# Optimization experiments

Hardware: AMD Instinct MI355X
Metric: run time of the kernel (lower is better)

The kernel has to match this reference:

```python
import jax, jax.numpy as jnp
import numpy as np

S, T, B = 50, 50, 64
SRC_V, TRG_V = 36616, 23262
E, EH, DH = 300, 512, 1024


def setup_inputs() -> dict:
    key = jax.random.key(0)
    ks = jax.random.split(key, 20)
    n = lambda k, shape: jax.random.normal(k, shape, jnp.float32) * 0.05
    return {
        "train_src_batch": jax.random.randint(ks[0], (S, B), 0, SRC_V),
        "train_trg_batch": jax.random.randint(ks[1], (T, B), 0, TRG_V),
        "emb_en": n(ks[2], (SRC_V, E)),
        "emb_de": n(ks[3], (TRG_V, E)),
        "enc_W_ih_f": n(ks[4], (4 * EH, E)),
        "enc_W_hh_f": n(ks[5], (4 * EH, EH)),
        "enc_b_f": n(ks[6], (4 * EH,)),
        "enc_W_ih_b": n(ks[7], (4 * EH, E)),
        "enc_W_hh_b": n(ks[8], (4 * EH, EH)),
        "enc_b_b": n(ks[9], (4 * EH,)),
        "dec_W_ih": n(ks[10], (4 * DH, E + DH)),
        "dec_W_hh": n(ks[11], (4 * DH, DH)),
        "dec_b": n(ks[12], (4 * DH,)),
        "W_gen": n(ks[13], (TRG_V, DH)),
        "b_gen": n(ks[14], (TRG_V,)),
        "W_i": n(ks[15], (DH, DH)),
        "W_o": n(ks[16], (DH, 2 * DH)),
    }


def _lstm_step(x, h, c, W_ih, W_hh, b):
    # PyTorch gate order: i, f, g, o
    gates = x @ W_ih.T + h @ W_hh.T + b
    i, f, g, o = jnp.split(gates, 4, axis=-1)
    c_new = jax.nn.sigmoid(f) * c + jax.nn.sigmoid(i) * jnp.tanh(g)
    h_new = jax.nn.sigmoid(o) * jnp.tanh(c_new)
    return h_new, c_new


def _run_lstm(x_seq, W_ih, W_hh, b, hidden):
    h0 = jnp.zeros((x_seq.shape[1], hidden), x_seq.dtype)
    def step(carry, x):
        h, c = carry
        h, c = _lstm_step(x, h, c, W_ih, W_hh, b)
        return (h, c), h
    (h, c), hs = jax.lax.scan(step, (h0, h0), x_seq)
    return hs, h, c


def _forward(train_src_batch, train_trg_batch, emb_en, emb_de,
             enc_W_ih_f, enc_W_hh_f, enc_b_f, enc_W_ih_b, enc_W_hh_b, enc_b_b,
             dec_W_ih, dec_W_hh, dec_b, W_gen, b_gen, W_i, W_o):
    x = emb_en[train_src_batch]                       # [S,B,E]
    hs_f, hf, cf = _run_lstm(x, enc_W_ih_f, enc_W_hh_f, enc_b_f, EH)
    hs_b, hb, cb = _run_lstm(x[::-1], enc_W_ih_b, enc_W_hh_b, enc_b_b, EH)
    output_hs = jnp.concatenate([hs_f, hs_b[::-1]], axis=-1)  # [S,B,1024]
    # Faithful to h.contiguous().view(B,1024) on direction-major [2,B,512]
    h = jnp.reshape(jnp.stack([hf, hb], axis=0), (B, DH))
    c = jnp.reshape(jnp.stack([cf, cb], axis=0), (B, DH))

    emb_trg = emb_de[train_trg_batch[: T - 1]]        # [T-1,B,E]

    def step(carry, e):
        h, c = carry
        # score[j,b] = output_hs[j,b] . (W_i h[b])  (the diag of the original mm)
        scores = jnp.einsum('sbd,bd->sb', output_hs, h @ W_i.T)
        # legacy nn.Softmax() on 2D input -> softmax over dim=1 (batch axis)
        a = jax.nn.softmax(scores, axis=1)
        s_t = jnp.einsum('sb,sbd->bd', a, output_hs)
        c_t = jnp.tanh(jnp.concatenate([s_t, h], axis=1) @ W_o.T)
        dec_in = jnp.concatenate([c_t, e], axis=1)    # [B, 1024+300]
        h, c = _lstm_step(dec_in, h, c, dec_W_ih, dec_W_hh, dec_b)
        logp = jax.nn.log_softmax(h @ W_gen.T + b_gen, axis=1)
        return (h, c), logp

    _, outs = jax.lax.scan(step, (h, c), emb_trg)     # [T-1,B,V]
    out0 = jnp.zeros((1, B, TRG_V), outs.dtype)       # output[0] filled with 0
    return jnp.concatenate([out0, outs], axis=0)      # [T,B,V]


def reference(train_src_batch, train_trg_batch, emb_en, emb_de,
              enc_W_ih_f, enc_W_hh_f, enc_b_f, enc_W_ih_b, enc_W_hh_b, enc_b_b,
              dec_W_ih, dec_W_hh, dec_b, W_gen, b_gen, W_i, W_o):
    return _forward(train_src_batch, train_trg_batch, emb_en, emb_de,
                    enc_W_ih_f, enc_W_hh_f, enc_b_f, enc_W_ih_b, enc_W_hh_b, enc_b_b,
                    dec_W_ih, dec_W_hh, dec_b, W_gen, b_gen, W_i, W_o)
```

## Files before the change

kernel.cpp:

```cpp
#include <hip/hip_runtime.h>
#include <hip/hip_bf16.h>

#define SS 50
#define TT 50
#define BB 64
#define TRGV 23262
#define EE 300
#define EH 512
#define DH 1024

#define GMRE 3136
#define GMP 3200
#define GK 1024
#define GNRE TRGV
#define GNP 23296

typedef short bf16x8 __attribute__((ext_vector_type(8)));
typedef float f32x4 __attribute__((ext_vector_type(4)));

__device__ __forceinline__ void glds16(const void* g, void* l) {
  __builtin_amdgcn_global_load_lds(
      (const __attribute__((address_space(1))) void*)g,
      (__attribute__((address_space(3))) void*)l, 16, 0, 0);
}

__device__ __forceinline__ float sigm(float x) { return 1.f / (1.f + expf(-x)); }
__device__ __forceinline__ float sum4(f32x4 v) { return v[0] + v[1] + v[2] + v[3]; }
__device__ __forceinline__ float bfu2f(unsigned short u) {
  unsigned int x = ((unsigned)u) << 16;
  return __uint_as_float(x);
}

__device__ __forceinline__ void split2(float x, __hip_bfloat16& hi, __hip_bfloat16& lo) {
  hi = __float2bfloat16(x);
  lo = __float2bfloat16(x - __bfloat162float(hi));
}

__device__ __forceinline__ void gbarg(unsigned* arrive, unsigned* gen,
                                      int idxInGrp, int n, bool poller) {
  __syncthreads();
  unsigned g = __hip_atomic_load(gen, __ATOMIC_RELAXED, __HIP_MEMORY_SCOPE_AGENT);
  if (threadIdx.x == 0)
    __hip_atomic_store(arrive + idxInGrp, g + 1u, __ATOMIC_RELEASE, __HIP_MEMORY_SCOPE_AGENT);
  if (poller) {
    int i = threadIdx.x;
    if (i < n) {
      while (__hip_atomic_load(arrive + i, __ATOMIC_RELAXED, __HIP_MEMORY_SCOPE_AGENT) < g + 1u)
        __builtin_amdgcn_s_sleep(1);
      (void)__hip_atomic_load(arrive + i, __ATOMIC_ACQUIRE, __HIP_MEMORY_SCOPE_AGENT);
    }
    __syncthreads();
    if (threadIdx.x == 0)
      __hip_atomic_store(gen, g + 1u, __ATOMIC_RELEASE, __HIP_MEMORY_SCOPE_AGENT);
  }
  if (threadIdx.x == 0) {
    while (__hip_atomic_load(gen, __ATOMIC_RELAXED, __HIP_MEMORY_SCOPE_AGENT) < g + 1u)
      __builtin_amdgcn_s_sleep(1);
    (void)__hip_atomic_load(gen, __ATOMIC_ACQUIRE, __HIP_MEMORY_SCOPE_AGENT);
  }
  __syncthreads();
}

__global__ void k_zero(float* __restrict__ p, long n) {
  long i = (long)blockIdx.x * 256 + threadIdx.x;
  if (i < n) p[i] = 0.f;
}
__global__ void k_zero_bf(__hip_bfloat16* __restrict__ p, long n) {
  long i = (long)blockIdx.x * 256 + threadIdx.x;
  if (i < n) p[i] = __float2bfloat16(0.f);
}

__global__ void k_embed(const int* __restrict__ src, const float* __restrict__ emb,
                        float* __restrict__ x) {
  int id = blockIdx.x * 256 + threadIdx.x;
  if (id >= SS * BB * EE) return;
  int sb = id / EE, e = id % EE;
  x[id] = emb[(long)src[sb] * EE + e];
}

__global__ void k_dbperm(const float* __restrict__ db, float* __restrict__ dbp) {
  int id = blockIdx.x * 256 + threadIdx.x;
  if (id >= 4096) return;
  int u = id >> 2, g = id & 3;
  dbp[id] = db[g * 1024 + u];
}

__global__ void k_split_pad(const float* __restrict__ in, int ld_in, int col_off,
                            int Kreal, int Kpad, int rows_real, long rows_pad,
                            int mode, __hip_bfloat16* __restrict__ out) {
  long id = (long)blockIdx.x * 256 + threadIdx.x;
  if (id >= rows_pad * Kpad) return;
  long r = id / Kpad;
  int k = id % Kpad;
  float v = 0.f;
  if (r < rows_real && k < Kreal) {
    if (mode == 3) {
      v = in[(long)k * ld_in + col_off + r];
    } else {
      long sr = r;
      if (mode == 1) sr = ((49 - (r >> 6)) << 6) + (r & 63);
      else if (mode == 2) sr = (long)(r & 3) * 1024 + (r >> 2);
      v = in[sr * ld_in + col_off + k];
    }
  }
  __hip_bfloat16 hi, lo;
  split2(v, hi, lo);
  out[r * 2 * Kpad + k] = hi;
  out[r * 2 * Kpad + Kpad + k] = lo;
}

__global__ void k_embgather_split(const int* __restrict__ trg, const float* __restrict__ emb,
                                  __hip_bfloat16* __restrict__ out) {
  long id = (long)blockIdx.x * 256 + threadIdx.x;
  if (id >= 3200L * 320) return;
  long r = id / 320;
  int k = id % 320;
  int t = r >> 6, b = r & 63;
  float v = 0.f;
  if (t < TT - 1 && k < EE) v = emb[(long)trg[t * BB + b] * EE + k];
  __hip_bfloat16 hi, lo;
  split2(v, hi, lo);
  out[r * 640 + k] = hi;
  out[r * 640 + 320 + k] = lo;
}

__global__ void k_tobf16_pad(const float* __restrict__ W, __hip_bfloat16* __restrict__ Wb,
                             long nrow_real, long nrow_pad, int K) {
  long id = (long)blockIdx.x * 256 + threadIdx.x;
  if (id >= nrow_pad * K) return;
  long r = id / K;
  Wb[id] = __float2bfloat16(r < nrow_real ? W[id] : 0.f);
}

__global__ void k_repackT(const float* __restrict__ in, float* __restrict__ out) {
  long id = (long)blockIdx.x * 256 + threadIdx.x;
  if (id >= 3200L * 1024) return;
  long r = id >> 10;
  int n = id & 1023;
  out[((long)(n >> 2) * 3200 + r) * 4 + (n & 3)] = in[id];
}

template<int OUTBF>
__global__ __launch_bounds__(256) void k_gsplit(
    const __hip_bfloat16* __restrict__ A2, const __hip_bfloat16* __restrict__ W2,
    const float* __restrict__ bias, void* __restrict__ Cout,
    int Mreal, int Nreal, int ldc, int Kpad) {
  __shared__ __hip_bfloat16 As[128 * 32];
  __shared__ __hip_bfloat16 Bs[128 * 32];
  int tid = threadIdx.x, lane = tid & 63, w = tid >> 6;
  long m0 = (long)blockIdx.y * 128, n0 = (long)blockIdx.x * 128;
  int lda2 = 2 * Kpad;
  int srow = lane >> 2;
  int scol = (lane & 3) * 8;
  char* lA0 = (char*)As + w * 2048;
  char* lA1 = lA0 + 1024;
  char* lB0 = (char*)Bs + w * 2048;
  char* lB1 = lB0 + 1024;
  int wm = (w >> 1) * 64, wn = (w & 1) * 64;
  int fr = lane & 15;
  int kc = (lane >> 4) * 8;
  f32x4 acc[4][4] = {};

  for (int seg = 0; seg < 3; ++seg) {
    const __hip_bfloat16* Ab = A2 + (seg == 1 ? Kpad : 0);
    const __hip_bfloat16* Wb = W2 + (seg == 2 ? Kpad : 0);
    const __hip_bfloat16* gA0 = Ab + (m0 + w * 32 + srow) * (long)lda2 + scol;
    const __hip_bfloat16* gA1 = gA0 + 16L * lda2;
    const __hip_bfloat16* gB0 = Wb + (n0 + w * 32 + srow) * (long)lda2 + scol;
    const __hip_bfloat16* gB1 = gB0 + 16L * lda2;
    for (int kt = 0; kt < Kpad / 32; ++kt) {
      int k0 = kt * 32;
      glds16(gA0 + k0, lA0);
      glds16(gA1 + k0, lA1);
      glds16(gB0 + k0, lB0);
      glds16(gB1 + k0, lB1);
      __syncthreads();
      bf16x8 a[4], b[4];
      for (int mi = 0; mi < 4; ++mi)
        a[mi] = *(const bf16x8*)(As + (wm + mi * 16 + fr) * 32 + kc);
      for (int ni = 0; ni < 4; ++ni)
        b[ni] = *(const bf16x8*)(Bs + (wn + ni * 16 + fr) * 32 + kc);
      for (int mi = 0; mi < 4; ++mi)
        for (int ni = 0; ni < 4; ++ni)
          acc[mi][ni] = __builtin_amdgcn_mfma_f32_16x16x32_bf16(a[mi], b[ni], acc[mi][ni], 0, 0, 0);
      __syncthreads();
    }
  }

  for (int mi = 0; mi < 4; ++mi) {
    for (int ni = 0; ni < 4; ++ni) {
      int n = (int)n0 + wn + ni * 16 + (lane & 15);
      if (n >= Nreal) continue;
      float bv = bias ? bias[n] : 0.f;
      for (int r = 0; r < 4; ++r) {
        int m = (int)m0 + wm + mi * 16 + (lane >> 4) * 4 + r;
        if (m >= Mreal) continue;
        float v = acc[mi][ni][r] + bv;
        if (OUTBF) ((__hip_bfloat16*)Cout)[(long)m * ldc + n] = __float2bfloat16(v);
        else ((float*)Cout)[(long)m * ldc + n] = v;
      }
    }
  }
}

__global__ __launch_bounds__(512) void persist_enc(
    const float* __restrict__ xW_f, const float* __restrict__ xW_b,
    const float* __restrict__ Whf, const float* __restrict__ Whb,
    float* __restrict__ hs, float* hA, float* hB, float* hA2, float* hB2,
    float* __restrict__ cf, float* __restrict__ cb,
    float* __restrict__ hd0, float* __restrict__ hT0, float* __restrict__ cdD,
    unsigned* __restrict__ bar) {
  __shared__ float WL[16 * 516];
  int t = threadIdx.x;
  int blk = blockIdx.x;
  int dir = blk >> 7, bl = blk & 127;
  const float* Whh = dir ? Whb : Whf;
  const float* xWb0 = dir ? xW_b : xW_f;
  float* c = dir ? cb : cf;
  float* hp = dir ? hA2 : hA;
  float* hn = dir ? hB2 : hB;
  unsigned* arrG = bar + dir * 128;
  unsigned* genG = bar + 784 + dir * 16;
  unsigned* arrA = bar + 256;
  unsigned* genA = bar + 816;

  for (int idx = t; idx < 16 * 512; idx += 512) {
    int r = idx >> 9, k = idx & 511;
    int srcrow = (r & 3) * 512 + (bl * 4 + (r >> 2));
    WL[r * 516 + k] = Whh[(long)srcrow * 512 + k];
  }
  __syncthreads();

  int j = t & 15;
  int b0 = t >> 4, b1 = b0 + 32;
  int g = j & 3;
  int ju = bl * 4 + (j >> 2);
  int lbase = (t & 63) & ~3;
  const f32x4* wq = (const f32x4*)(WL + j * 516);

  for (int s = 0; s < SS; ++s) {
    const f32x4* h0q = (const f32x4*)(hp + b0 * 512);
    const f32x4* h1q = (const f32x4*)(hp + b1 * 512);
    f32x4 v0 = {0, 0, 0, 0}, v1 = {0, 0, 0, 0};
    for (int q = 0; q < 128; ++q) {
      f32x4 wv = wq[q];
      v0 += wv * h0q[q];
      v1 += wv * h1q[q];
    }
    const float* xW = xWb0 + (long)(s * BB) * 2048;
    float a0 = sum4(v0) + xW[b0 * 2048 + g * 512 + ju];
    float a1 = sum4(v1) + xW[b1 * 2048 + g * 512 + ju];
    float gi0 = __shfl(a0, lbase + 0), gf0 = __shfl(a0, lbase + 1);
    float gg0 = __shfl(a0, lbase + 2), go0 = __shfl(a0, lbase + 3);
    float gi1 = __shfl(a1, lbase + 0), gf1 = __shfl(a1, lbase + 1);
    float gg1 = __shfl(a1, lbase + 2), go1 = __shfl(a1, lbase + 3);
    if ((t & 3) == 0) {
      int hscol = dir ? (512 + ju) : ju;
      int srow = dir ? (SS - 1 - s) : s;
      long hsrow0 = (long)(srow * BB + b0) * DH + hscol;
      long hsrow1 = (long)(srow * BB + b1) * DH + hscol;
      float cn0 = sigm(gf0) * c[b0 * 512 + ju] + sigm(gi0) * tanhf(gg0);
      float hn0 = sigm(go0) * tanhf(cn0);
      c[b0 * 512 + ju] = cn0;
      hn[b0 * 512 + ju] = hn0;
      hs[hsrow0] = hn0;
      float cn1 = sigm(gf1) * c[b1 * 512 + ju] + sigm(gi1) * tanhf(gg1);
      float hn1 = sigm(go1) * tanhf(cn1);
      c[b1 * 512 + ju] = cn1;
      hn[b1 * 512 + ju] = hn1;
      hs[hsrow1] = hn1;
    }
    float* tmp = hp; hp = hn; hn = tmp;
    gbarg(arrG, genG, bl, 128, bl == 0);
  }
  gbarg(arrA, genA, blk, 256, blk == 0);
  int gid = blk * 512 + t;
  if (gid < 65536) {
    int d2 = gid >> 15, b = (gid >> 9) & 63, j2 = gid & 511;
    float hv = (d2 ? hA2 : hA)[b * 512 + j2];
    float cv = (d2 ? cb : cf)[b * 512 + j2];
    hd0[gid] = hv;
    cdD[gid] = cv;
    int bp = gid >> 10, jp = gid & 1023;
    hT0[jp * 64 + bp] = hv;
  }
}

__global__ __launch_bounds__(1024) void persist_dec(
    const float* __restrict__ G, const float* __restrict__ HsWo1T,
    const float* __restrict__ Wo, const float* __restrict__ dWih,
    const float* __restrict__ dWhh, const __hip_bfloat16* __restrict__ Eg,
    float* hd0, float* hd1, float* hT0, float* hT1,
    float* __restrict__ cd, float* __restrict__ attw, float* __restrict__ ctb,
    __hip_bfloat16* __restrict__ A_bf, unsigned* __restrict__ bar) {
  __shared__ float WcL[16 * 2052];
  __shared__ __hip_bfloat16 WoLi[1024 * 4];
  __shared__ float red[4096];
  int t = threadIdx.x;
  int blk = blockIdx.x;
  int w = t >> 6, lane = t & 63;
  int j = t & 15, b = t >> 4;
  unsigned* arrive = bar + 512;
  unsigned* gen = bar + 832;

  for (int idx = t; idx < 16 * 2048; idx += 1024) {
    int r = idx >> 11, k = idx & 2047;
    int rp2 = blk * 16 + r;
    long srcrow = (long)(rp2 & 3) * 1024 + (rp2 >> 2);
    float v = (k < 1024) ? dWih[srcrow * 1324 + k] : dWhh[srcrow * 1024 + (k - 1024)];
    WcL[r * 2052 + k] = v;
  }
  for (int idx = t; idx < 4 * 1024; idx += 1024) {
    int r = idx >> 10, k = idx & 1023;
    WoLi[k * 4 + r] = __float2bfloat16(Wo[(long)(blk * 4 + r) * 2048 + 1024 + k]);
  }
  __syncthreads();

  float* hcur = hd0; float* hnew = hd1;
  float* hTc = hT0;  float* hTn = hT1;
  int rp = blk * 16 + j;
  int ju = blk * 4 + (j >> 2);
  int lbase = (t & 63) & ~3;
  const f32x4* hw4 = (const f32x4*)(HsWo1T + (long)blk * 3200 * 4);
  f32x4* red4 = (f32x4*)red;

  for (int ts = 0; ts < TT - 1; ++ts) {
    float eg = bfu2f(((const unsigned short*)Eg)[((long)(ts * BB + b)) * 4096 + rp]);
    f32x4 z1 = {0, 0, 0, 0};
    for (int k = w * 64; k < w * 64 + 64; ++k) {
      float hb = hTc[k * 64 + lane];
      const unsigned short* wv4 = (const unsigned short*)(WoLi + k * 4);
      f32x4 wv = {bfu2f(wv4[0]), bfu2f(wv4[1]), bfu2f(wv4[2]), bfu2f(wv4[3])};
      z1 += hb * wv;
    }
    if (blk < SS) {
      int s = blk;
      const f32x4* gq = (const f32x4*)(G + ((long)(s * BB + lane)) * DH + w * 64);
      const f32x4* hq = (const f32x4*)(hcur + lane * DH + w * 64);
      f32x4 a4 = {0, 0, 0, 0};
      for (int q = 0; q < 16; ++q) a4 += gq[q] * hq[q];
      red[w * 64 + lane] = sum4(a4);
      __syncthreads();
      if (t < 64) {
        float sc = 0.f;
        for (int i = 0; i < 16; ++i) sc += red[i * 64 + t];
        float m = sc;
        for (int o = 32; o > 0; o >>= 1) m = fmaxf(m, __shfl_xor(m, o));
        float e = expf(sc - m);
        float su = e;
        for (int o = 32; o > 0; o >>= 1) su += __shfl_xor(su, o);
        attw[s * BB + t] = e / su;
      }
      __syncthreads();
    }
    red4[w * 64 + lane] = z1;
    gbarg(arrive, gen, blk, 256, blk == 0);

    {
      f32x4 z2 = {0, 0, 0, 0};
      for (int s = w; s < SS; s += 16) {
        float aw = attw[s * BB + lane];
        z2 += aw * hw4[s * 64 + lane];
      }
      red4[w * 64 + lane] += z2;
      __syncthreads();
      if (t < 256) {
        int bb = t >> 2, nl = t & 3;
        float sv = 0.f;
        for (int i = 0; i < 16; ++i) sv += red[(i * 64 + bb) * 4 + nl];
        ctb[bb * DH + blk * 4 + nl] = tanhf(sv);
      }
    }
    gbarg(arrive, gen, blk, 256, blk == 0);

    {
      const f32x4* wq1 = (const f32x4*)(WcL + j * 2052);
      const f32x4* wq2 = (const f32x4*)(WcL + j * 2052 + 1024);
      const f32x4* c0q = (const f32x4*)(ctb + b * DH);
      const f32x4* h0q = (const f32x4*)(hcur + b * DH);
      f32x4 v0 = {0, 0, 0, 0};
      #pragma unroll 8
      for (int q = 0; q < 256; ++q) v0 += wq1[q] * c0q[q];
      #pragma unroll 8
      for (int q = 0; q < 256; ++q) v0 += wq2[q] * h0q[q];
      float a0 = sum4(v0) + eg;
      float gi0 = __shfl(a0, lbase + 0), gf0 = __shfl(a0, lbase + 1);
      float gg0 = __shfl(a0, lbase + 2), go0 = __shfl(a0, lbase + 3);
      if ((t & 3) == 0) {
        float cn0 = sigm(gf0) * cd[b * DH + ju] + sigm(gi0) * tanhf(gg0);
        float hn0 = sigm(go0) * tanhf(cn0);
        cd[b * DH + ju] = cn0;
        hnew[b * DH + ju] = hn0;
        hTn[ju * 64 + b] = hn0;
        A_bf[(long)ts * (BB * DH) + b * DH + ju] = __float2bfloat16(hn0);
      }
    }
    { float* x = hcur; hcur = hnew; hnew = x; }
    { float* x = hTc; hTc = hTn; hTn = x; }
    gbarg(arrive, gen, blk, 256, blk == 0);
  }
}

__global__ __launch_bounds__(256) void k_gen_mfma(
    const __hip_bfloat16* __restrict__ A, const __hip_bfloat16* __restrict__ Bw,
    const float* __restrict__ bias, float* __restrict__ C) {
  __shared__ __hip_bfloat16 As[128 * 32];
  __shared__ __hip_bfloat16 Bs[128 * 32];
  int tid = threadIdx.x;
  int lane = tid & 63, w = tid >> 6;
  long m0 = (long)blockIdx.y * 128, n0 = (long)blockIdx.x * 128;
  int srow = lane >> 2;
  int scol = (lane & 3) * 8;
  const __hip_bfloat16* gA0 = A + (m0 + w * 32 + srow) * GK + scol;
  const __hip_bfloat16* gA1 = gA0 + 16 * GK;
  const __hip_bfloat16* gB0 = Bw + (n0 + w * 32 + srow) * GK + scol;
  const __hip_bfloat16* gB1 = gB0 + 16 * GK;
  char* lA0 = (char*)As + w * 2048;
  char* lA1 = lA0 + 1024;
  char* lB0 = (char*)Bs + w * 2048;
  char* lB1 = lB0 + 1024;
  int wm = (w >> 1) * 64, wn = (w & 1) * 64;
  int fr = lane & 15;
  int kc = (lane >> 4) * 8;
  f32x4 acc[4][4] = {};
  for (int kt = 0; kt < GK / 32; ++kt) {
    int k0 = kt * 32;
    glds16(gA0 + k0, lA0);
    glds16(gA1 + k0, lA1);
    glds16(gB0 + k0, lB0);
    glds16(gB1 + k0, lB1);
    __syncthreads();
    bf16x8 a[4], b[4];
    for (int mi = 0; mi < 4; ++mi)
      a[mi] = *(const bf16x8*)(As + (wm + mi * 16 + fr) * 32 + kc);
    for (int ni = 0; ni < 4; ++ni)
      b[ni] = *(const bf16x8*)(Bs + (wn + ni * 16 + fr) * 32 + kc);
    for (int mi = 0; mi < 4; ++mi)
      for (int ni = 0; ni < 4; ++ni)
        acc[mi][ni] = __builtin_amdgcn_mfma_f32_16x16x32_bf16(a[mi], b[ni], acc[mi][ni], 0, 0, 0);
    __syncthreads();
  }
  for (int mi = 0; mi < 4; ++mi) {
    for (int ni = 0; ni < 4; ++ni) {
      int n = (int)n0 + wn + ni * 16 + (lane & 15);
      if (n >= GNRE) continue;
      float bv = bias[n];
      for (int r = 0; r < 4; ++r) {
        int m = (int)m0 + wm + mi * 16 + (lane >> 4) * 4 + r;
        if (m < GMRE) C[(long)m * TRGV + n] = acc[mi][ni][r] + bv;
      }
    }
  }
}

__global__ __launch_bounds__(256) void k_logsoftmax(float* __restrict__ out) {
  int r = blockIdx.x;
  float* p = out + (long)(BB + r) * TRGV;
  int tid = threadIdx.x;
  __shared__ float red[256];
  float m = -1e30f;
  for (int i = tid; i < TRGV; i += 256) m = fmaxf(m, p[i]);
  red[tid] = m;
  __syncthreads();
  for (int s = 128; s > 0; s >>= 1) {
    if (tid < s) red[tid] = fmaxf(red[tid], red[tid + s]);
    __syncthreads();
  }
  m = red[0];
  __syncthreads();
  float sum = 0.f;
  for (int i = tid; i < TRGV; i += 256) sum += expf(p[i] - m);
  red[tid] = sum;
  __syncthreads();
  for (int s = 128; s > 0; s >>= 1) {
    if (tid < s) red[tid] += red[tid + s];
    __syncthreads();
  }
  float lse = m + logf(red[0]);
  for (int i = tid; i < TRGV; i += 256) p[i] -= lse;
}

extern "C" void kernel_launch(void* const* d_in, const int* in_sizes, int n_in,
                              void* d_out, int out_size, void* d_ws, size_t ws_size,
                              hipStream_t stream) {
  const int* src = (const int*)d_in[0];
  const int* trg = (const int*)d_in[1];
  const float* emb_en = (const float*)d_in[2];
  const float* emb_de = (const float*)d_in[3];
  const float* eWih_f = (const float*)d_in[4];
  const float* eWhh_f = (const float*)d_in[5];
  const float* eb_f = (const float*)d_in[6];
  const float* eWih_b = (const float*)d_in[7];
  const float* eWhh_b = (const float*)d_in[8];
  const float* eb_b = (const float*)d_in[9];
  const float* dWih = (const float*)d_in[10];
  const float* dWhh = (const float*)d_in[11];
  const float* db = (const float*)d_in[12];
  const float* Wgen = (const float*)d_in[13];
  const float* bgen = (const float*)d_in[14];
  const float* Wi = (const float*)d_in[15];
  const float* Wo = (const float*)d_in[16];
  float* out = (float*)d_out;

  float* base = (float*)d_ws;
  __hip_bfloat16* xsf = (__hip_bfloat16*)base;
  __hip_bfloat16* xsb = (__hip_bfloat16*)(base + 1024000);
  __hip_bfloat16* Wihf2 = (__hip_bfloat16*)(base + 2048000);
  __hip_bfloat16* Wihb2 = (__hip_bfloat16*)(base + 2703360);
  float* xW_f = base + 3358720;
  float* xW_b = base + 9912320;
  __hip_bfloat16* hs2 = (__hip_bfloat16*)base;
  __hip_bfloat16* Wi2 = (__hip_bfloat16*)(base + 3276800);
  __hip_bfloat16* Wo12 = (__hip_bfloat16*)(base + 4325376);
  __hip_bfloat16* eg2 = (__hip_bfloat16*)(base + 5373952);
  __hip_bfloat16* Wce2 = (__hip_bfloat16*)(base + 6397952);
  __hip_bfloat16* E_g = (__hip_bfloat16*)(base + 7708672);
  __hip_bfloat16* Wgen_bf = (__hip_bfloat16*)base;
  float* p = base + 16465920;
  float* x_enc = p; p += SS * BB * EE;
  float* hs = p; p += (long)SS * BB * DH;
  float* G = p; p += (long)SS * BB * DH;
  float* HsWo1 = p; p += (long)SS * BB * DH;
  float* HsWo1T = p; p += (long)SS * BB * DH;
  __hip_bfloat16* A_bf = (__hip_bfloat16*)p; p += (GMP * GK) / 2;
  float* dbp = p; p += 4096;
  float* attw = p; p += SS * BB;
  float* hd0 = p; p += BB * DH;
  float* hd1 = p; p += BB * DH;
  float* hT0 = p; p += BB * DH;
  float* hT1 = p; p += BB * DH;
  float* cd = p; p += BB * DH;
  float* ctb = p; p += BB * DH;
  float* hA = p; p += BB * EH;
  float* hB = p; p += BB * EH;
  float* hA2 = p; p += BB * EH;
  float* hB2 = p; p += BB * EH;
  float* cf = p; p += BB * EH;
  float* cb = p; p += BB * EH;
  unsigned* bar = (unsigned*)p; p += 1024;

  dim3 b256(256);

  k_embed<<<dim3((SS * BB * EE + 255) / 256), b256, 0, stream>>>(src, emb_en, x_enc);
  k_zero<<<dim3((6 * BB * EH + 255) / 256), b256, 0, stream>>>(hA, 6 * BB * EH);
  k_zero<<<dim3(4), b256, 0, stream>>>((float*)bar, 1024);
  k_zero<<<dim3((int)(((long)BB * TRGV + 255) / 256)), b256, 0, stream>>>(out, (long)BB * TRGV);
  k_zero_bf<<<dim3(((GMP - GMRE) * GK + 255) / 256), b256, 0, stream>>>(
      A_bf + (long)GMRE * GK, (long)(GMP - GMRE) * GK);
  k_dbperm<<<dim3(16), b256, 0, stream>>>(db, dbp);

  k_split_pad<<<dim3((3200 * 320 + 255) / 256), b256, 0, stream>>>(
      x_enc, EE, 0, EE, 320, 3200, 3200, 0, xsf);
  k_split_pad<<<dim3((3200 * 320 + 255) / 256), b256, 0, stream>>>(
      x_enc, EE, 0, EE, 320, 3200, 3200, 1, xsb);
  k_split_pad<<<dim3((2048 * 320 + 255) / 256), b256, 0, stream>>>(
      eWih_f, EE, 0, EE, 320, 2048, 2048, 0, Wihf2);
  k_split_pad<<<dim3((2048 * 320 + 255) / 256), b256, 0, stream>>>(
      eWih_b, EE, 0, EE, 320, 2048, 2048, 0, Wihb2);
  k_gsplit<0><<<dim3(16, 25), b256, 0, stream>>>(xsf, Wihf2, eb_f, xW_f, 3200, 2048, 2048, 320);
  k_gsplit<0><<<dim3(16, 25), b256, 0, stream>>>(xsb, Wihb2, eb_b, xW_b, 3200, 2048, 2048, 320);

  {
    void* args[] = {(void*)&xW_f, (void*)&xW_b, (void*)&eWhh_f, (void*)&eWhh_b,
                    (void*)&hs, (void*)&hA, (void*)&hB, (void*)&hA2, (void*)&hB2,
                    (void*)&cf, (void*)&cb, (void*)&hd0, (void*)&hT0, (void*)&cd,
                    (void*)&bar};
    hipLaunchCooperativeKernel((const void*)persist_enc, dim3(256), dim3(512),
                               args, 0, stream);
  }

  k_split_pad<<<dim3((int)((3200L * 1024 + 255) / 256)), b256, 0, stream>>>(
      hs, DH, 0, DH, 1024, 3200, 3200, 0, hs2);
  k_split_pad<<<dim3((int)((1024L * 1024 + 255) / 256)), b256, 0, stream>>>(
      Wi, DH, 0, DH, 1024, 1024, 1024, 3, Wi2);
  k_split_pad<<<dim3((int)((1024L * 1024 + 255) / 256)), b256, 0, stream>>>(
      Wo, 2 * DH, 0, DH, 1024, 1024, 1024, 0, Wo12);
  k_embgather_split<<<dim3((int)((3200L * 320 + 255) / 256)), b256, 0, stream>>>(
      trg, emb_de, eg2);
  k_split_pad<<<dim3((int)((4096L * 320 + 255) / 256)), b256, 0, stream>>>(
      dWih, 1324, 1024, EE, 320, 4096, 4096, 2, Wce2);
  k_gsplit<0><<<dim3(8, 25), b256, 0, stream>>>(hs2, Wi2, (const float*)nullptr, G, 3200, 1024, 1024, 1024);
  k_gsplit<0><<<dim3(8, 25), b256, 0, stream>>>(hs2, Wo12, (const float*)nullptr, HsWo1, 3200, 1024, 1024, 1024);
  k_repackT<<<dim3((int)((3200L * 1024 + 255) / 256)), b256, 0, stream>>>(HsWo1, HsWo1T);
  k_gsplit<1><<<dim3(32, 25), b256, 0, stream>>>(eg2, Wce2, dbp, E_g, 3136, 4096, 4096, 320);

  {
    void* args[] = {(void*)&G, (void*)&HsWo1T, (void*)&Wo, (void*)&dWih, (void*)&dWhh,
                    (void*)&E_g, (void*)&hd0, (void*)&hd1, (void*)&hT0, (void*)&hT1,
                    (void*)&cd, (void*)&attw, (void*)&ctb, (void*)&A_bf, (void*)&bar};
    hipLaunchCooperativeKernel((const void*)persist_dec, dim3(256), dim3(1024),
                               args, 0, stream);
  }

  k_tobf16_pad<<<dim3((int)(((long)GNP * GK + 255) / 256)), b256, 0, stream>>>(
      Wgen, Wgen_bf, GNRE, GNP, GK);
  k_gen_mfma<<<dim3(GNP / 128, GMP / 128), b256, 0, stream>>>(
      A_bf, Wgen_bf, bgen, out + (long)BB * TRGV);
  k_logsoftmax<<<dim3((TT - 1) * BB), b256, 0, stream>>>(out);
}
```

Before: 7.882 ms.

## Use split-bf16 MFMA for decoder LSTM gates and restructure attention scores

The decoder's per-step LSTM gate matvec, previously fp32 FMA over LDS weights, becomes bf16x3-style split (hi/lo) MFMA 16x16x32 with the weights pre-split into LDS and activations staged through global_load_lds. Attention scores are now computed per batch row, using a batch-major repack of G and shuffle reductions. Softmax moves into the post-barrier context phase, so one intra-block sync phase disappears. The hi/lo split buffers for c_t and h are double-buffered. The trade-offs are extra repack and split work, many __syncthreads inside the MFMA loop, and reading the Wo slice directly from global memory instead of LDS.

```diff
diff --git a/kernel.cpp b/kernel.cpp
--- a/kernel.cpp
+++ b/kernel.cpp
@@ -26,10 +26,6 @@
 
 __device__ __forceinline__ float sigm(float x) { return 1.f / (1.f + expf(-x)); }
 __device__ __forceinline__ float sum4(f32x4 v) { return v[0] + v[1] + v[2] + v[3]; }
-__device__ __forceinline__ float bfu2f(unsigned short u) {
-  unsigned int x = ((unsigned)u) << 16;
-  return __uint_as_float(x);
-}
 
 __device__ __forceinline__ void split2(float x, __hip_bfloat16& hi, __hip_bfloat16& lo) {
   hi = __float2bfloat16(x);
@@ -138,6 +134,16 @@
   long r = id >> 10;
   int n = id & 1023;
   out[((long)(n >> 2) * 3200 + r) * 4 + (n & 3)] = in[id];
+}
+
+__global__ void k_repackG(const float* __restrict__ in, float* __restrict__ out) {
+  long id = (long)blockIdx.x * 256 + threadIdx.x;
+  if (id >= 3200L * 1024) return;
+  long b = id / 51200;
+  long r = id % 51200;
+  long s = r >> 10;
+  int d = r & 1023;
+  out[id] = in[((long)s * 64 + b) * 1024 + d];
 }
 
 template<int OUTBF>
@@ -209,7 +215,7 @@
     float* __restrict__ hs, float* hA, float* hB, float* hA2, float* hB2,
     float* __restrict__ cf, float* __restrict__ cb,
     float* __restrict__ hd0, float* __restrict__ hT0, float* __restrict__ cdD,
-    unsigned* __restrict__ bar) {
+    __hip_bfloat16* __restrict__ x2A, unsigned* __restrict__ bar) {
   __shared__ float WL[16 * 516];
   int t = threadIdx.x;
   int blk = blockIdx.x;
@@ -283,116 +289,151 @@
     cdD[gid] = cv;
     int bp = gid >> 10, jp = gid & 1023;
     hT0[jp * 64 + bp] = hv;
+    __hip_bfloat16 hi, lo;
+    split2(hv, hi, lo);
+    x2A[bp * 4096 + 1024 + jp] = hi;
+    x2A[bp * 4096 + 3072 + jp] = lo;
   }
 }
 
 __global__ __launch_bounds__(1024) void persist_dec(
-    const float* __restrict__ G, const float* __restrict__ HsWo1T,
+    const float* __restrict__ Gb, const float* __restrict__ HsWo1T,
     const float* __restrict__ Wo, const float* __restrict__ dWih,
     const float* __restrict__ dWhh, const __hip_bfloat16* __restrict__ Eg,
     float* hd0, float* hd1, float* hT0, float* hT1,
-    float* __restrict__ cd, float* __restrict__ attw, float* __restrict__ ctb,
-    __hip_bfloat16* __restrict__ A_bf, unsigned* __restrict__ bar) {
-  __shared__ float WcL[16 * 2052];
-  __shared__ __hip_bfloat16 WoLi[1024 * 4];
-  __shared__ float red[4096];
+    float* __restrict__ cd, float* __restrict__ scoresG,
+    __hip_bfloat16* __restrict__ A_bf,
+    __hip_bfloat16* __restrict__ xA, __hip_bfloat16* __restrict__ xB,
+    unsigned* __restrict__ bar) {
+  __shared__ __hip_bfloat16 WB[16 * 4096];
+  __shared__ float Abuf[4096];
   int t = threadIdx.x;
   int blk = blockIdx.x;
   int w = t >> 6, lane = t & 63;
-  int j = t & 15, b = t >> 4;
   unsigned* arrive = bar + 512;
   unsigned* gen = bar + 832;
 
   for (int idx = t; idx < 16 * 2048; idx += 1024) {
-    int r = idx >> 11, k = idx & 2047;
-    int rp2 = blk * 16 + r;
+    int jj = idx >> 11;
+    int k = idx & 2047;
+    int rp2 = blk * 16 + jj;
     long srcrow = (long)(rp2 & 3) * 1024 + (rp2 >> 2);
     float v = (k < 1024) ? dWih[srcrow * 1324 + k] : dWhh[srcrow * 1024 + (k - 1024)];
-    WcL[r * 2052 + k] = v;
-  }
-  for (int idx = t; idx < 4 * 1024; idx += 1024) {
-    int r = idx >> 10, k = idx & 1023;
-    WoLi[k * 4 + r] = __float2bfloat16(Wo[(long)(blk * 4 + r) * 2048 + 1024 + k]);
+    __hip_bfloat16 hi, lo;
+    split2(v, hi, lo);
+    WB[((k >> 3) * 16 + jj) * 8 + (k & 7)] = hi;
+    WB[(((k + 2048) >> 3) * 16 + jj) * 8 + (k & 7)] = lo;
   }
   __syncthreads();
 
   float* hcur = hd0; float* hnew = hd1;
   float* hTc = hT0;  float* hTn = hT1;
+  int j = t & 15, b = t >> 4;
   int rp = blk * 16 + j;
   int ju = blk * 4 + (j >> 2);
   int lbase = (t & 63) & ~3;
   const f32x4* hw4 = (const f32x4*)(HsWo1T + (long)blk * 3200 * 4);
-  f32x4* red4 = (f32x4*)red;
+  f32x4* Abuf4 = (f32x4*)Abuf;
+  int mt = w & 3, kg = w >> 2;
+  int row_a = mt * 16 + (lane & 15), kq = lane >> 4;
+  int s_ks = t >> 8, s_kq = (t >> 6) & 3, s_row = t & 63;
+  const float* wo2 = Wo + (long)(blk * 4) * 2048 + 1024;
 
   for (int ts = 0; ts < TT - 1; ++ts) {
-    float eg = bfu2f(((const unsigned short*)Eg)[((long)(ts * BB + b)) * 4096 + rp]);
-    f32x4 z1 = {0, 0, 0, 0};
-    for (int k = w * 64; k < w * 64 + 64; ++k) {
-      float hb = hTc[k * 64 + lane];
-      const unsigned short* wv4 = (const unsigned short*)(WoLi + k * 4);
-      f32x4 wv = {bfu2f(wv4[0]), bfu2f(wv4[1]), bfu2f(wv4[2]), bfu2f(wv4[3])};
-      z1 += hb * wv;
-    }
-    if (blk < SS) {
-      int s = blk;
-      const f32x4* gq = (const f32x4*)(G + ((long)(s * BB + lane)) * DH + w * 64);
-      const f32x4* hq = (const f32x4*)(hcur + lane * DH + w * 64);
-      f32x4 a4 = {0, 0, 0, 0};
-      for (int q = 0; q < 16; ++q) a4 += gq[q] * hq[q];
-      red[w * 64 + lane] = sum4(a4);
-      __syncthreads();
-      if (t < 64) {
-        float sc = 0.f;
-        for (int i = 0; i < 16; ++i) sc += red[i * 64 + t];
+    const __hip_bfloat16* xc = (ts & 1) ? xB : xA;
+    __hip_bfloat16* xn = (ts & 1) ? xA : xB;
+    float eg = __bfloat162float(Eg[((long)(ts * BB + b)) * 4096 + rp]);
+
+    if (blk < BB) {
+      int sp = t >> 4, cc = t & 15;
+      if (sp < SS) {
+        const f32x4* gq = (const f32x4*)(Gb + (long)blk * 51200 + sp * 1024 + cc * 64);
+        const f32x4* hq = (const f32x4*)(hcur + blk * DH + cc * 64);
+        f32x4 a4 = {0, 0, 0, 0};
+        #pragma unroll
+        for (int q = 0; q < 16; ++q) a4 += gq[q] * hq[q];
+        float p = sum4(a4);
+        p += __shfl_xor(p, 1);
+        p += __shfl_xor(p, 2);
+        p += __shfl_xor(p, 4);
+        p += __shfl_xor(p, 8);
+        if (cc == 0) scoresG[sp * 64 + blk] = p;
+      }
+    }
+    {
+      f32x4 z1 = {0, 0, 0, 0};
+      for (int k = w * 64; k < w * 64 + 64; ++k) {
+        float hb = hTc[k * 64 + lane];
+        f32x4 wv = {wo2[k], wo2[2048 + k], wo2[4096 + k], wo2[6144 + k]};
+        z1 += hb * wv;
+      }
+      Abuf4[w * 64 + lane] = z1;
+    }
+    gbarg(arrive, gen, blk, 256, blk == 0);
+
+    {
+      f32x4 z2 = {0, 0, 0, 0};
+      for (int s = w; s < SS; s += 16) {
+        float sc = scoresG[s * 64 + lane];
         float m = sc;
         for (int o = 32; o > 0; o >>= 1) m = fmaxf(m, __shfl_xor(m, o));
         float e = expf(sc - m);
         float su = e;
         for (int o = 32; o > 0; o >>= 1) su += __shfl_xor(su, o);
-        attw[s * BB + t] = e / su;
-      }
-      __syncthreads();
-    }
-    red4[w * 64 + lane] = z1;
-    gbarg(arrive, gen, blk, 256, blk == 0);
-
-    {
-      f32x4 z2 = {0, 0, 0, 0};
-      for (int s = w; s < SS; s += 16) {
-        float aw = attw[s * BB + lane];
-        z2 += aw * hw4[s * 64 + lane];
-      }
-      red4[w * 64 + lane] += z2;
+        z2 += (e / su) * hw4[s * 64 + lane];
+      }
+      Abuf4[w * 64 + lane] += z2;
       __syncthreads();
       if (t < 256) {
         int bb = t >> 2, nl = t & 3;
         float sv = 0.f;
-        for (int i = 0; i < 16; ++i) sv += red[(i * 64 + bb) * 4 + nl];
-        ctb[bb * DH + blk * 4 + nl] = tanhf(sv);
+        for (int i = 0; i < 16; ++i) sv += Abuf[(i * 64 + bb) * 4 + nl];
+        float ct = tanhf(sv);
+        __hip_bfloat16 hi, lo;
+        split2(ct, hi, lo);
+        xn = xn;
+        ((__hip_bfloat16*)xc)[bb * 4096 + blk * 4 + nl] = hi;
+        ((__hip_bfloat16*)xc)[bb * 4096 + 2048 + blk * 4 + nl] = lo;
       }
     }
     gbarg(arrive, gen, blk, 256, blk == 0);
 
     {
-      const f32x4* wq1 = (const f32x4*)(WcL + j * 2052);
-      const f32x4* wq2 = (const f32x4*)(WcL + j * 2052 + 1024);
-      const f32x4* c0q = (const f32x4*)(ctb + b * DH);
-      const f32x4* h0q = (const f32x4*)(hcur + b * DH);
-      f32x4 v0 = {0, 0, 0, 0};
-      #pragma unroll 8
-      for (int q = 0; q < 256; ++q) v0 += wq1[q] * c0q[q];
-      #pragma unroll 8
-      for (int q = 0; q < 256; ++q) v0 += wq2[q] * h0q[q];
-      float a0 = sum4(v0) + eg;
-      float gi0 = __shfl(a0, lbase + 0), gf0 = __shfl(a0, lbase + 1);
-      float gg0 = __shfl(a0, lbase + 2), go0 = __shfl(a0, lbase + 3);
+      f32x4 acc = {0, 0, 0, 0};
+      for (int seg = 0; seg < 3; ++seg) {
+        int aoff = (seg == 1) ? 2048 : 0;
+        int woff = (seg == 2) ? 2048 : 0;
+        for (int c = 0; c < 16; ++c) {
+          int k0 = c * 128;
+          glds16(xc + (long)s_row * 4096 + aoff + k0 + s_ks * 32 + s_kq * 8,
+                 (char*)Abuf + t * 16);
+          __syncthreads();
+          bf16x8 a = *(const bf16x8*)((__hip_bfloat16*)Abuf + kg * 2048 + kq * 512 + row_a * 8);
+          int gidx = ((woff + k0 + kg * 32) >> 3) + kq;
+          bf16x8 bfr = *(const bf16x8*)(WB + gidx * 128 + (lane & 15) * 8);
+          acc = __builtin_amdgcn_mfma_f32_16x16x32_bf16(a, bfr, acc, 0, 0, 0);
+          __syncthreads();
+        }
+      }
+      for (int r = 0; r < 4; ++r) {
+        int row = mt * 16 + kq * 4 + r;
+        Abuf[kg * 1024 + row * 16 + (lane & 15)] = acc[r];
+      }
+      __syncthreads();
+      float gv = Abuf[t] + Abuf[1024 + t] + Abuf[2048 + t] + Abuf[3072 + t] + eg;
+      float gi0 = __shfl(gv, lbase + 0), gf0 = __shfl(gv, lbase + 1);
+      float gg0 = __shfl(gv, lbase + 2), go0 = __shfl(gv, lbase + 3);
       if ((t & 3) == 0) {
         float cn0 = sigm(gf0) * cd[b * DH + ju] + sigm(gi0) * tanhf(gg0);
         float hn0 = sigm(go0) * tanhf(cn0);
         cd[b * DH + ju] = cn0;
         hnew[b * DH + ju] = hn0;
         hTn[ju * 64 + b] = hn0;
-        A_bf[(long)ts * (BB * DH) + b * DH + ju] = __float2bfloat16(hn0);
+        __hip_bfloat16 hi, lo;
+        split2(hn0, hi, lo);
+        A_bf[(long)ts * (BB * DH) + b * DH + ju] = hi;
+        xn[b * 4096 + 1024 + ju] = hi;
+        xn[b * 4096 + 3072 + ju] = lo;
       }
     }
     { float* x = hcur; hcur = hnew; hnew = x; }
@@ -520,17 +561,19 @@
   float* x_enc = p; p += SS * BB * EE;
   float* hs = p; p += (long)SS * BB * DH;
   float* G = p; p += (long)SS * BB * DH;
+  float* Gb = p; p += (long)SS * BB * DH;
   float* HsWo1 = p; p += (long)SS * BB * DH;
   float* HsWo1T = p; p += (long)SS * BB * DH;
   __hip_bfloat16* A_bf = (__hip_bfloat16*)p; p += (GMP * GK) / 2;
+  __hip_bfloat16* x2A = (__hip_bfloat16*)p; p += (BB * 4096) / 2;
+  __hip_bfloat16* x2B = (__hip_bfloat16*)p; p += (BB * 4096) / 2;
   float* dbp = p; p += 4096;
-  float* attw = p; p += SS * BB;
+  float* scoresG = p; p += SS * BB;
   float* hd0 = p; p += BB * DH;
   float* hd1 = p; p += BB * DH;
   float* hT0 = p; p += BB * DH;
   float* hT1 = p; p += BB * DH;
   float* cd = p; p += BB * DH;
-  float* ctb = p; p += BB * DH;
   float* hA = p; p += BB * EH;
   float* hB = p; p += BB * EH;
   float* hA2 = p; p += BB * EH;
@@ -564,7 +607,7 @@
     void* args[] = {(void*)&xW_f, (void*)&xW_b, (void*)&eWhh_f, (void*)&eWhh_b,
                     (void*)&hs, (void*)&hA, (void*)&hB, (void*)&hA2, (void*)&hB2,
                     (void*)&cf, (void*)&cb, (void*)&hd0, (void*)&hT0, (void*)&cd,
-                    (void*)&bar};
+                    (void*)&x2A, (void*)&bar};
     hipLaunchCooperativeKernel((const void*)persist_enc, dim3(256), dim3(512),
                                args, 0, stream);
   }
@@ -581,13 +624,15 @@
       dWih, 1324, 1024, EE, 320, 4096, 4096, 2, Wce2);
   k_gsplit<0><<<dim3(8, 25), b256, 0, stream>>>(hs2, Wi2, (const float*)nullptr, G, 3200, 1024, 1024, 1024);
   k_gsplit<0><<<dim3(8, 25), b256, 0, stream>>>(hs2, Wo12, (const float*)nullptr, HsWo1, 3200, 1024, 1024, 1024);
+  k_repackG<<<dim3((int)((3200L * 1024 + 255) / 256)), b256, 0, stream>>>(G, Gb);
   k_repackT<<<dim3((int)((3200L * 1024 + 255) / 256)), b256, 0, stream>>>(HsWo1, HsWo1T);
   k_gsplit<1><<<dim3(32, 25), b256, 0, stream>>>(eg2, Wce2, dbp, E_g, 3136, 4096, 4096, 320);
 
   {
-    void* args[] = {(void*)&G, (void*)&HsWo1T, (void*)&Wo, (void*)&dWih, (void*)&dWhh,
+    void* args[] = {(void*)&Gb, (void*)&HsWo1T, (void*)&Wo, (void*)&dWih, (void*)&dWhh,
                     (void*)&E_g, (void*)&hd0, (void*)&hd1, (void*)&hT0, (void*)&hT1,
-                    (void*)&cd, (void*)&attw, (void*)&ctb, (void*)&A_bf, (void*)&bar};
+                    (void*)&cd, (void*)&scoresG, (void*)&A_bf, (void*)&x2A, (void*)&x2B,
+                    (void*)&bar};
     hipLaunchCooperativeKernel((const void*)persist_dec, dim3(256), dim3(1024),
                                args, 0, stream);
   }
```

New measurement: 6.669 ms. -15.4%, faster.
